# Kernel tuning notes

Measured on AMD Instinct MI355X. Metric: run time of the kernel, lower is better.

Reference implementation:

```python
import jax, jax.numpy as jnp
import numpy as np

B, H, L, D = 4, 16, 2048, 64
NEG = -1e9  # large negative for masked positions


def setup_inputs() -> dict:
    key = jax.random.key(0)
    kq, kk, kv, km, kb = jax.random.split(key, 5)
    Q = jax.random.normal(kq, (B, H, L, D), dtype=jnp.float32)
    K = jax.random.normal(kk, (B, H, L, D), dtype=jnp.float32)
    V = jax.random.normal(kv, (B, H, L, D), dtype=jnp.float32)
    attention_mask = jax.random.randint(km, (B, L), 0, 2, dtype=jnp.int32)
    attention_bias = jax.random.normal(kb, (B, L, L), dtype=jnp.float32)
    return {"Q": Q, "K": K, "V": V, "attention_mask": attention_mask,
            "attention_bias": attention_bias}


def reference(Q, K, V, attention_mask, attention_bias):
    scale = Q.shape[-1] ** 0.5
    # (b,h,l,l) = Q @ K^T / sqrt(d)
    score = jnp.einsum("bhqd,bhkd->bhqk", Q, K) / jnp.float32(scale)
    # bias (b,l,l) broadcasts over heads
    score = score + attention_bias[:, None, :, :]
    # mask (b,l): 1 valid, 0 invalid -> mask out key positions
    valid = attention_mask[:, None, None, :].astype(jnp.bool_)
    score = jnp.where(valid, score, jnp.float32(NEG))
    weight = jax.nn.softmax(score, axis=-1)
    # dropout p=0.0 -> identity
    return jnp.einsum("bhqk,bhkd->bhqd", weight, V)
```

## Files before the change

### kernel.cpp

```cpp
#include <hip/hip_runtime.h>


constexpr int kH = 16;
constexpr int kL = 2048;
constexpr int kD = 64;

typedef __attribute__((ext_vector_type(8))) short bf16x8;
typedef __attribute__((ext_vector_type(4))) float f32x4;

constexpr float kQScale = 0.125f * 1.44269504088896340736f;
constexpr float kL2E    = 1.44269504088896340736f;
constexpr float kNegBig = -1e9f;

__device__ __forceinline__ unsigned short f2bf(float f) {
  unsigned u = __float_as_uint(f);
  u += 0x7FFF + ((u >> 16) & 1);
  return (unsigned short)(u >> 16);
}
__device__ __forceinline__ unsigned pack2(float a, float b) {
  return (unsigned)f2bf(a) | ((unsigned)f2bf(b) << 16);
}
__device__ __forceinline__ unsigned cvt_pk_bf16(float lo, float hi) {
  unsigned r;
  asm("v_cvt_pk_bf16_f32 %0, %1, %2" : "=v"(r) : "v"(lo), "v"(hi));
  return r;
}
__device__ __forceinline__ float exp2_hw(float x) {
  float r; asm("v_exp_f32 %0, %1" : "=v"(r) : "v"(x)); return r;
}

__global__ __launch_bounds__(256, 2)
void attn_fwd(const float* __restrict__ Qg, const float* __restrict__ Kg,
              const float* __restrict__ Vg, const int* __restrict__ maskg,
              const float* __restrict__ biasg, float* __restrict__ outg) {
  __shared__ __align__(16) char smem[39936];
  unsigned short* const KsBase = (unsigned short*)smem;
  unsigned short* const VtBase = (unsigned short*)(smem + 9216);
  unsigned short* const QsAll  = (unsigned short*)smem;

  const int tid  = threadIdx.x;
  const int lane = tid & 63;
  const int w    = tid >> 6;
  const int col  = lane & 15;
  const int quad = lane >> 4;

  const int wg = blockIdx.x + (blockIdx.y << 4) + (blockIdx.z << 7);
  const int sw = ((wg & 7) << 6) | (wg >> 3);
  const int h  = sw & 15;
  const int qb = (sw >> 4) & 7;
  const int b  = sw >> 7;
  const int q0 = qb * 256;

  unsigned short* const Ps = (unsigned short*)(smem + 19456) + w * 2560;

  const size_t bh = (size_t)b * kH + h;
  const float4* const Q4 = (const float4*)(Qg + (bh * kL + q0) * kD);
  const float4* const K4 = (const float4*)(Kg + bh * kL * kD);
  const float4* const V4 = (const float4*)(Vg + bh * kL * kD);
  const float*  const brow = biasg + (size_t)b * kL * kL;
  const int*    const mrow = maskg + b * kL;

#pragma unroll
  for (int i = 0; i < 16; ++i) {
    const int slot = tid + i * 256;
    const int row = slot >> 4, dc = slot & 15;
    const float4 v = Q4[slot];
    *(uint2*)&QsAll[row * 72 + dc * 4] =
        make_uint2(cvt_pk_bf16(v.x * kQScale, v.y * kQScale),
                   cvt_pk_bf16(v.z * kQScale, v.w * kQScale));
  }
  __syncthreads();
  bf16x8 qf[4][2];
#pragma unroll
  for (int qt = 0; qt < 4; ++qt)
#pragma unroll
    for (int kc = 0; kc < 2; ++kc)
      qf[qt][kc] = *(const bf16x8*)
          &QsAll[(w * 64 + qt * 16 + col) * 72 + kc * 32 + quad * 8];
  __syncthreads();

  const int keyA = tid >> 4, dcA = tid & 15;
  const int jp   = tid >> 4, dcv = tid & 15;

  {
    const float4 a  = K4[keyA * 16 + dcA];
    const float4 c  = K4[(16 + keyA) * 16 + dcA];
    const float4 v0 = V4[(2 * jp) * 16 + dcv];
    const float4 v1 = V4[(2 * jp + 1) * 16 + dcv];
    *(uint2*)&KsBase[keyA * 72 + dcA * 4] =
        make_uint2(cvt_pk_bf16(a.x, a.y), cvt_pk_bf16(a.z, a.w));
    *(uint2*)&KsBase[(keyA + 16) * 72 + dcA * 4] =
        make_uint2(cvt_pk_bf16(c.x, c.y), cvt_pk_bf16(c.z, c.w));
    *(unsigned*)&VtBase[(dcv * 4 + 0) * 40 + 2 * jp] = pack2(v0.x, v1.x);
    *(unsigned*)&VtBase[(dcv * 4 + 1) * 40 + 2 * jp] = pack2(v0.y, v1.y);
    *(unsigned*)&VtBase[(dcv * 4 + 2) * 40 + 2 * jp] = pack2(v0.z, v1.z);
    *(unsigned*)&VtBase[(dcv * 4 + 3) * 40 + 2 * jp] = pack2(v0.w, v1.w);
  }

  f32x4 oacc[4][5];
  const f32x4 z4 = {0.f, 0.f, 0.f, 0.f};
#pragma unroll
  for (int qt = 0; qt < 4; ++qt)
#pragma unroll
    for (int dt = 0; dt < 5; ++dt) oacc[qt][dt] = z4;

  bf16x8 vones;
#pragma unroll
  for (int i = 0; i < 8; ++i) vones[i] = (short)0x3F80;

  const float* const bb =
      brow + (size_t)(q0 + w * 64 + quad * 4) * kL + col;

  for (int t = 0; t < 64; ++t) {
    const int buf = t & 1;
    const int k0 = t * 32;
    unsigned short* const Ks = KsBase + buf * 2304;
    unsigned short* const Vt = VtBase + buf * 2560;

    float4 pk0, pk1, pv0, pv1;
    const bool pf = (t < 63);
    if (pf) {
      const int kn = k0 + 32;
      pk0 = K4[(kn + keyA) * 16 + dcA];
      pk1 = K4[(kn + 16 + keyA) * 16 + dcA];
      pv0 = V4[(kn + 2 * jp) * 16 + dcv];
      pv1 = V4[(kn + 2 * jp + 1) * 16 + dcv];
    }

    const int mk0 = mrow[k0 + col];
    const int mk1 = mrow[k0 + 16 + col];
    const float sel0 = mk0 ? kL2E : 0.f, add0 = mk0 ? 0.f : kNegBig;
    const float sel1 = mk1 ? kL2E : 0.f, add1 = mk1 ? 0.f : kNegBig;
    float bt[4][4][2];
#pragma unroll
    for (int qt = 0; qt < 4; ++qt)
#pragma unroll
      for (int r = 0; r < 4; ++r) {
        const float* bp = bb + (size_t)(qt * 16 + r) * kL + k0;
        bt[qt][r][0] = fmaf(bp[0], sel0, add0);
        bt[qt][r][1] = fmaf(bp[16], sel1, add1);
      }

    __syncthreads();

    f32x4 sacc[4][2];
#pragma unroll
    for (int qt = 0; qt < 4; ++qt) { sacc[qt][0] = z4; sacc[qt][1] = z4; }
#pragma unroll
    for (int kc = 0; kc < 2; ++kc) {
      const bf16x8 bk0 = *(const bf16x8*)&Ks[col * 72 + kc * 32 + quad * 8];
      const bf16x8 bk1 = *(const bf16x8*)&Ks[(16 + col) * 72 + kc * 32 + quad * 8];
#pragma unroll
      for (int qt = 0; qt < 4; ++qt) {
        sacc[qt][0] = __builtin_amdgcn_mfma_f32_16x16x32_bf16(
            qf[qt][kc], bk0, sacc[qt][0], 0, 0, 0);
        sacc[qt][1] = __builtin_amdgcn_mfma_f32_16x16x32_bf16(
            qf[qt][kc], bk1, sacc[qt][1], 0, 0, 0);
      }
    }

#pragma unroll
    for (int qt = 0; qt < 4; ++qt)
#pragma unroll
      for (int r = 0; r < 4; ++r) {
        const float p0 = exp2_hw(sacc[qt][0][r] + bt[qt][r][0]);
        const float p1 = exp2_hw(sacc[qt][1][r] + bt[qt][r][1]);
        const int prow = (qt * 16 + quad * 4 + r) * 40;
        Ps[prow + col]      = (unsigned short)((__float_as_uint(p0) + 0x8000) >> 16);
        Ps[prow + 16 + col] = (unsigned short)((__float_as_uint(p1) + 0x8000) >> 16);
      }
    asm volatile("" ::: "memory");

    bf16x8 ap[4];
#pragma unroll
    for (int qt = 0; qt < 4; ++qt)
      ap[qt] = *(const bf16x8*)&Ps[(qt * 16 + col) * 40 + quad * 8];
#pragma unroll
    for (int dt = 0; dt < 4; ++dt) {
      const bf16x8 bv = *(const bf16x8*)&Vt[(dt * 16 + col) * 40 + quad * 8];
#pragma unroll
      for (int qt = 0; qt < 4; ++qt)
        oacc[qt][dt] = __builtin_amdgcn_mfma_f32_16x16x32_bf16(
            ap[qt], bv, oacc[qt][dt], 0, 0, 0);
    }
#pragma unroll
    for (int qt = 0; qt < 4; ++qt)
      oacc[qt][4] = __builtin_amdgcn_mfma_f32_16x16x32_bf16(
          ap[qt], vones, oacc[qt][4], 0, 0, 0);

    if (pf) {
      unsigned short* const Ksn = KsBase + (buf ^ 1) * 2304;
      unsigned short* const Vtn = VtBase + (buf ^ 1) * 2560;
      *(uint2*)&Ksn[keyA * 72 + dcA * 4] =
          make_uint2(cvt_pk_bf16(pk0.x, pk0.y), cvt_pk_bf16(pk0.z, pk0.w));
      *(uint2*)&Ksn[(keyA + 16) * 72 + dcA * 4] =
          make_uint2(cvt_pk_bf16(pk1.x, pk1.y), cvt_pk_bf16(pk1.z, pk1.w));
      *(unsigned*)&Vtn[(dcv * 4 + 0) * 40 + 2 * jp] = pack2(pv0.x, pv1.x);
      *(unsigned*)&Vtn[(dcv * 4 + 1) * 40 + 2 * jp] = pack2(pv0.y, pv1.y);
      *(unsigned*)&Vtn[(dcv * 4 + 2) * 40 + 2 * jp] = pack2(pv0.z, pv1.z);
      *(unsigned*)&Vtn[(dcv * 4 + 3) * 40 + 2 * jp] = pack2(pv0.w, pv1.w);
    }
  }

  float* const orow = outg + (bh * kL + q0) * kD;
#pragma unroll
  for (int qt = 0; qt < 4; ++qt)
#pragma unroll
    for (int r = 0; r < 4; ++r) {
      const float li = 1.0f / oacc[qt][4][r];
      float* op = orow + (size_t)(w * 64 + qt * 16 + quad * 4 + r) * kD + col;
#pragma unroll
      for (int dt = 0; dt < 4; ++dt)
        op[dt * 16] = oacc[qt][dt][r] * li;
    }
}

extern "C" void kernel_launch(void* const* d_in, const int* in_sizes, int n_in,
                              void* d_out, int out_size, void* d_ws, size_t ws_size,
                              hipStream_t stream) {
  const float* Q    = (const float*)d_in[0];
  const float* K    = (const float*)d_in[1];
  const float* V    = (const float*)d_in[2];
  const int*   mask = (const int*)d_in[3];
  const float* bias = (const float*)d_in[4];
  float* out = (float*)d_out;

  dim3 grid(kH, kL / 256, 4);
  dim3 block(256);
  attn_fwd<<<grid, block, 0, stream>>>(Q, K, V, mask, bias, out);
}
```

Measured before the change: 284.4 us.

## Pre-convert K/V to bf16 workspace and stream tiles via global_load_lds

Adds a prep kernel that converts K and V to bf16 once per (b,h) and lays out K with padding and V transposed in a global workspace. The attention kernel then stages each 32-key tile straight into LDS with global_load_lds, removing the per-block fp32 loads, conversion and transpose. Q blocks shrink to 128 rows with occupancy 4, which doubles the number of workgroups. The cost is an extra launch and workspace traffic, plus more bias reads per key tile spread across more blocks. A fallback kernel keeps the old path when the workspace is too small.

```diff
diff --git a/kernel.cpp b/kernel.cpp
--- a/kernel.cpp
+++ b/kernel.cpp
@@ -4,6 +4,7 @@
 constexpr int kH = 16;
 constexpr int kL = 2048;
 constexpr int kD = 64;
+constexpr size_t kWsNeed = (size_t)64 * 64 * 10240;
 
 typedef __attribute__((ext_vector_type(8))) short bf16x8;
 typedef __attribute__((ext_vector_type(4))) float f32x4;
@@ -29,14 +30,47 @@
   float r; asm("v_exp_f32 %0, %1" : "=v"(r) : "v"(x)); return r;
 }
 
-__global__ __launch_bounds__(256, 2)
-void attn_fwd(const float* __restrict__ Qg, const float* __restrict__ Kg,
-              const float* __restrict__ Vg, const int* __restrict__ maskg,
-              const float* __restrict__ biasg, float* __restrict__ outg) {
-  __shared__ __align__(16) char smem[39936];
-  unsigned short* const KsBase = (unsigned short*)smem;
-  unsigned short* const VtBase = (unsigned short*)(smem + 9216);
-  unsigned short* const QsAll  = (unsigned short*)smem;
+__global__ __launch_bounds__(256)
+void prep_kv(const float* __restrict__ Kg, const float* __restrict__ Vg,
+             unsigned* __restrict__ ws) {
+  const int t  = blockIdx.x;
+  const int bh = blockIdx.y;
+  const int tid = threadIdx.x;
+  const float2* const K2 = (const float2*)(Kg + ((size_t)bh * kL + t * 32) * kD);
+  const float*  const Vp = Vg + ((size_t)bh * kL + t * 32) * kD;
+  unsigned* const wsK = ws + ((size_t)bh * 64 + t) * 2560;
+  unsigned* const wsV = wsK + 1280;
+#pragma unroll
+  for (int i = 0; i < 4; ++i) {
+    const int id = tid + i * 256;
+    const int kk = id >> 5, d2 = id & 31;
+    const float2 v = K2[kk * 32 + d2];
+    wsK[kk * 36 + d2] = cvt_pk_bf16(v.x, v.y);
+  }
+#pragma unroll
+  for (int i = 0; i < 4; ++i) {
+    const int id = tid + i * 256;
+    const int d = id >> 4, k2 = id & 15;
+    const float a = Vp[(2 * k2) * kD + d];
+    const float b = Vp[(2 * k2 + 1) * kD + d];
+    wsV[d * 20 + k2] = pack2(a, b);
+  }
+}
+
+__device__ __forceinline__ void stage_tile(char* lds, const char* g, int lane) {
+  __builtin_amdgcn_global_load_lds((const void*)(g + lane * 16),        (void*)(lds),        16, 0, 0);
+  __builtin_amdgcn_global_load_lds((const void*)(g + 1024 + lane * 16), (void*)(lds + 1024), 16, 0, 0);
+  __builtin_amdgcn_global_load_lds((const void*)(g + 2048 + lane * 4),  (void*)(lds + 2048),  4, 0, 0);
+  __builtin_amdgcn_global_load_lds((const void*)(g + 2304 + lane * 4),  (void*)(lds + 2304),  4, 0, 0);
+}
+
+__global__ __launch_bounds__(256, 4)
+void attn_fwd(const float* __restrict__ Qg, const int* __restrict__ maskg,
+              const float* __restrict__ biasg,
+              const char* __restrict__ wsg, float* __restrict__ outg) {
+  __shared__ __align__(16) char smem[30720];
+  unsigned short* const SB    = (unsigned short*)smem;
+  unsigned short* const QsAll = (unsigned short*)smem;
 
   const int tid  = threadIdx.x;
   const int lane = tid & 63;
@@ -44,22 +78,167 @@
   const int col  = lane & 15;
   const int quad = lane >> 4;
 
+  const int wg = blockIdx.x + (blockIdx.y << 4) + (blockIdx.z << 8);
+  const int sw = ((wg & 7) << 7) | (wg >> 3);
+  const int h  = sw & 15;
+  const int qb = (sw >> 4) & 15;
+  const int b  = sw >> 8;
+  const int q0 = qb * 128;
+
+  unsigned short* const Ps = (unsigned short*)(smem + 20480) + w * 1280;
+
+  const size_t bh = (size_t)b * kH + h;
+  const float4* const Q4 = (const float4*)(Qg + (bh * kL + q0) * kD);
+  const char*   const wsBH = wsg + (size_t)bh * 64 * 10240;
+  const float*  const brow = biasg + (size_t)b * kL * kL;
+  const int*    const mrow = maskg + b * kL;
+
+#pragma unroll
+  for (int i = 0; i < 8; ++i) {
+    const int slot = tid + i * 256;
+    const int row = slot >> 4, dc = slot & 15;
+    const float4 v = Q4[slot];
+    *(uint2*)&QsAll[row * 72 + dc * 4] =
+        make_uint2(cvt_pk_bf16(v.x * kQScale, v.y * kQScale),
+                   cvt_pk_bf16(v.z * kQScale, v.w * kQScale));
+  }
+  __syncthreads();
+  bf16x8 qf[2][2];
+#pragma unroll
+  for (int qt = 0; qt < 2; ++qt)
+#pragma unroll
+    for (int kc = 0; kc < 2; ++kc)
+      qf[qt][kc] = *(const bf16x8*)
+          &QsAll[(w * 32 + qt * 16 + col) * 72 + kc * 32 + quad * 8];
+  __syncthreads();
+
+  stage_tile(smem + w * 2560, wsBH + w * 2560, lane);
+
+  f32x4 oacc[2][5];
+  const f32x4 z4 = {0.f, 0.f, 0.f, 0.f};
+#pragma unroll
+  for (int qt = 0; qt < 2; ++qt)
+#pragma unroll
+    for (int dt = 0; dt < 5; ++dt) oacc[qt][dt] = z4;
+
+  bf16x8 vones;
+#pragma unroll
+  for (int i = 0; i < 8; ++i) vones[i] = (short)0x3F80;
+
+  const float* const bb =
+      brow + (size_t)(q0 + w * 32 + quad * 4) * kL + col;
+
+  for (int t = 0; t < 64; ++t) {
+    const int buf = t & 1;
+    const int k0 = t * 32;
+    unsigned short* const Ks = SB + buf * 5120;
+    unsigned short* const Vt = Ks + 2560;
+
+    const int mk0 = mrow[k0 + col];
+    const int mk1 = mrow[k0 + 16 + col];
+    const float sel0 = mk0 ? kL2E : 0.f, add0 = mk0 ? 0.f : kNegBig;
+    const float sel1 = mk1 ? kL2E : 0.f, add1 = mk1 ? 0.f : kNegBig;
+    float bt[2][4][2];
+#pragma unroll
+    for (int qt = 0; qt < 2; ++qt)
+#pragma unroll
+      for (int r = 0; r < 4; ++r) {
+        const float* bp = bb + (size_t)(qt * 16 + r) * kL + k0;
+        bt[qt][r][0] = fmaf(bp[0], sel0, add0);
+        bt[qt][r][1] = fmaf(bp[16], sel1, add1);
+      }
+
+    __syncthreads();
+
+    if (t < 63)
+      stage_tile(smem + (buf ^ 1) * 10240 + w * 2560,
+                 wsBH + (size_t)(t + 1) * 10240 + w * 2560, lane);
+
+    f32x4 sacc[2][2];
+#pragma unroll
+    for (int qt = 0; qt < 2; ++qt) { sacc[qt][0] = z4; sacc[qt][1] = z4; }
+#pragma unroll
+    for (int kc = 0; kc < 2; ++kc) {
+      const bf16x8 bk0 = *(const bf16x8*)&Ks[col * 72 + kc * 32 + quad * 8];
+      const bf16x8 bk1 = *(const bf16x8*)&Ks[(16 + col) * 72 + kc * 32 + quad * 8];
+#pragma unroll
+      for (int qt = 0; qt < 2; ++qt) {
+        sacc[qt][0] = __builtin_amdgcn_mfma_f32_16x16x32_bf16(
+            qf[qt][kc], bk0, sacc[qt][0], 0, 0, 0);
+        sacc[qt][1] = __builtin_amdgcn_mfma_f32_16x16x32_bf16(
+            qf[qt][kc], bk1, sacc[qt][1], 0, 0, 0);
+      }
+    }
+
+#pragma unroll
+    for (int qt = 0; qt < 2; ++qt)
+#pragma unroll
+      for (int r = 0; r < 4; ++r) {
+        const float p0 = exp2_hw(sacc[qt][0][r] + bt[qt][r][0]);
+        const float p1 = exp2_hw(sacc[qt][1][r] + bt[qt][r][1]);
+        const int prow = (qt * 16 + quad * 4 + r) * 40;
+        Ps[prow + col]      = (unsigned short)((__float_as_uint(p0) + 0x8000) >> 16);
+        Ps[prow + 16 + col] = (unsigned short)((__float_as_uint(p1) + 0x8000) >> 16);
+      }
+    asm volatile("" ::: "memory");
+
+    bf16x8 ap[2];
+#pragma unroll
+    for (int qt = 0; qt < 2; ++qt)
+      ap[qt] = *(const bf16x8*)&Ps[(qt * 16 + col) * 40 + quad * 8];
+#pragma unroll
+    for (int dt = 0; dt < 4; ++dt) {
+      const bf16x8 bv = *(const bf16x8*)&Vt[(dt * 16 + col) * 40 + quad * 8];
+#pragma unroll
+      for (int qt = 0; qt < 2; ++qt)
+        oacc[qt][dt] = __builtin_amdgcn_mfma_f32_16x16x32_bf16(
+            ap[qt], bv, oacc[qt][dt], 0, 0, 0);
+    }
+#pragma unroll
+    for (int qt = 0; qt < 2; ++qt)
+      oacc[qt][4] = __builtin_amdgcn_mfma_f32_16x16x32_bf16(
+          ap[qt], vones, oacc[qt][4], 0, 0, 0);
+  }
+
+  float* const orow = outg + (bh * kL + q0) * kD;
+#pragma unroll
+  for (int qt = 0; qt < 2; ++qt)
+#pragma unroll
+    for (int r = 0; r < 4; ++r) {
+      const float li = 1.0f / oacc[qt][4][r];
+      float* op = orow + (size_t)(w * 32 + qt * 16 + quad * 4 + r) * kD + col;
+#pragma unroll
+      for (int dt = 0; dt < 4; ++dt)
+        op[dt * 16] = oacc[qt][dt][r] * li;
+    }
+}
+
+__global__ __launch_bounds__(256, 2)
+void attn_fwd_fb(const float* __restrict__ Qg, const float* __restrict__ Kg,
+                 const float* __restrict__ Vg, const int* __restrict__ maskg,
+                 const float* __restrict__ biasg, float* __restrict__ outg) {
+  __shared__ __align__(16) char smem[39936];
+  unsigned short* const KsBase = (unsigned short*)smem;
+  unsigned short* const VtBase = (unsigned short*)(smem + 9216);
+  unsigned short* const QsAll  = (unsigned short*)smem;
+  const int tid  = threadIdx.x;
+  const int lane = tid & 63;
+  const int w    = tid >> 6;
+  const int col  = lane & 15;
+  const int quad = lane >> 4;
   const int wg = blockIdx.x + (blockIdx.y << 4) + (blockIdx.z << 7);
   const int sw = ((wg & 7) << 6) | (wg >> 3);
   const int h  = sw & 15;
   const int qb = (sw >> 4) & 7;
   const int b  = sw >> 7;
   const int q0 = qb * 256;
-
   unsigned short* const Ps = (unsigned short*)(smem + 19456) + w * 2560;
-
   const size_t bh = (size_t)b * kH + h;
   const float4* const Q4 = (const float4*)(Qg + (bh * kL + q0) * kD);
   const float4* const K4 = (const float4*)(Kg + bh * kL * kD);
   const float4* const V4 = (const float4*)(Vg + bh * kL * kD);
   const float*  const brow = biasg + (size_t)b * kL * kL;
   const int*    const mrow = maskg + b * kL;
-
 #pragma unroll
   for (int i = 0; i < 16; ++i) {
     const int slot = tid + i * 256;
@@ -78,10 +257,8 @@
       qf[qt][kc] = *(const bf16x8*)
           &QsAll[(w * 64 + qt * 16 + col) * 72 + kc * 32 + quad * 8];
   __syncthreads();
-
   const int keyA = tid >> 4, dcA = tid & 15;
   const int jp   = tid >> 4, dcv = tid & 15;
-
   {
     const float4 a  = K4[keyA * 16 + dcA];
     const float4 c  = K4[(16 + keyA) * 16 + dcA];
@@ -96,27 +273,22 @@
     *(unsigned*)&VtBase[(dcv * 4 + 2) * 40 + 2 * jp] = pack2(v0.z, v1.z);
     *(unsigned*)&VtBase[(dcv * 4 + 3) * 40 + 2 * jp] = pack2(v0.w, v1.w);
   }
-
   f32x4 oacc[4][5];
   const f32x4 z4 = {0.f, 0.f, 0.f, 0.f};
 #pragma unroll
   for (int qt = 0; qt < 4; ++qt)
 #pragma unroll
     for (int dt = 0; dt < 5; ++dt) oacc[qt][dt] = z4;
-
   bf16x8 vones;
 #pragma unroll
   for (int i = 0; i < 8; ++i) vones[i] = (short)0x3F80;
-
   const float* const bb =
       brow + (size_t)(q0 + w * 64 + quad * 4) * kL + col;
-
   for (int t = 0; t < 64; ++t) {
     const int buf = t & 1;
     const int k0 = t * 32;
     unsigned short* const Ks = KsBase + buf * 2304;
     unsigned short* const Vt = VtBase + buf * 2560;
-
     float4 pk0, pk1, pv0, pv1;
     const bool pf = (t < 63);
     if (pf) {
@@ -126,7 +298,6 @@
       pv0 = V4[(kn + 2 * jp) * 16 + dcv];
       pv1 = V4[(kn + 2 * jp + 1) * 16 + dcv];
     }
-
     const int mk0 = mrow[k0 + col];
     const int mk1 = mrow[k0 + 16 + col];
     const float sel0 = mk0 ? kL2E : 0.f, add0 = mk0 ? 0.f : kNegBig;
@@ -140,9 +311,7 @@
         bt[qt][r][0] = fmaf(bp[0], sel0, add0);
         bt[qt][r][1] = fmaf(bp[16], sel1, add1);
       }
-
     __syncthreads();
-
     f32x4 sacc[4][2];
 #pragma unroll
     for (int qt = 0; qt < 4; ++qt) { sacc[qt][0] = z4; sacc[qt][1] = z4; }
@@ -158,7 +327,6 @@
             qf[qt][kc], bk1, sacc[qt][1], 0, 0, 0);
       }
     }
-
 #pragma unroll
     for (int qt = 0; qt < 4; ++qt)
 #pragma unroll
@@ -170,7 +338,6 @@
         Ps[prow + 16 + col] = (unsigned short)((__float_as_uint(p1) + 0x8000) >> 16);
       }
     asm volatile("" ::: "memory");
-
     bf16x8 ap[4];
 #pragma unroll
     for (int qt = 0; qt < 4; ++qt)
@@ -187,7 +354,6 @@
     for (int qt = 0; qt < 4; ++qt)
       oacc[qt][4] = __builtin_amdgcn_mfma_f32_16x16x32_bf16(
           ap[qt], vones, oacc[qt][4], 0, 0, 0);
-
     if (pf) {
       unsigned short* const Ksn = KsBase + (buf ^ 1) * 2304;
       unsigned short* const Vtn = VtBase + (buf ^ 1) * 2560;
@@ -201,7 +367,6 @@
       *(unsigned*)&Vtn[(dcv * 4 + 3) * 40 + 2 * jp] = pack2(pv0.w, pv1.w);
     }
   }
-
   float* const orow = outg + (bh * kL + q0) * kD;
 #pragma unroll
   for (int qt = 0; qt < 4; ++qt)
@@ -225,7 +390,12 @@
   const float* bias = (const float*)d_in[4];
   float* out = (float*)d_out;
 
-  dim3 grid(kH, kL / 256, 4);
-  dim3 block(256);
-  attn_fwd<<<grid, block, 0, stream>>>(Q, K, V, mask, bias, out);
-}
+  if (ws_size >= kWsNeed && d_ws != nullptr) {
+    prep_kv<<<dim3(64, 64), dim3(256), 0, stream>>>(K, V, (unsigned*)d_ws);
+    attn_fwd<<<dim3(kH, kL / 128, 4), dim3(256), 0, stream>>>(
+        Q, mask, bias, (const char*)d_ws, out);
+  } else {
+    attn_fwd_fb<<<dim3(kH, kL / 256, 4), dim3(256), 0, stream>>>(
+        Q, K, V, mask, bias, out);
+  }
+}
```

Measured after the change: 301.7 us. 6.1% more time.
